# Optimization experiments

Measured on AMD Instinct MI355X. Metric: run time of the kernel, lower is better.

Reference implementation:

```python
import jax, jax.numpy as jnp
import numpy as np

FIELD_NUM = 40
EMBED_DIM = 64
BATCH = 2048

# pair indices matching itertools.combinations(range(F), 2) order
_I, _J = np.triu_indices(FIELD_NUM, k=1)
PAIR_I = jnp.asarray(_I)
PAIR_J = jnp.asarray(_J)


def setup_inputs() -> dict:
    key = jax.random.key(0)
    k1, k2 = jax.random.split(key)
    inputs = jax.random.normal(k1, (BATCH, FIELD_NUM, EMBED_DIM), dtype=jnp.float32)
    # glorot_normal for square [D, D] weight: std = sqrt(2 / (D + D)) = sqrt(1/D)
    w = jax.random.normal(k2, (EMBED_DIM, EMBED_DIM), dtype=jnp.float32) * (1.0 / EMBED_DIM) ** 0.5
    return {"inputs": inputs, "w": w}


def reference(inputs, w):
    # inputs: [B, F, D], w: [D, D]
    # bilinear_type='all': p_{ij} = (v_i @ W) * v_j for all i<j, concat on feature axis
    xw = jnp.einsum("bfd,de->bfe", inputs, w)          # [B, F, D] (one GEMM, shared W)
    p = xw[:, PAIR_I, :] * inputs[:, PAIR_J, :]          # [B, P, D], P = F*(F-1)/2
    B = inputs.shape[0]
    return p.reshape(B, -1)                               # [B, P*D] == tf.concat(p, axis=1)
```

## Files before the change

kernel.cpp:

```cpp
#include <hip/hip_runtime.h>

#define FNUM 40
#define DIM  64
#define NPAIR 780
#define BLOCK 256
#define IN4   (FNUM * DIM / 4)
#define OUT4  (NPAIR * DIM / 4)

typedef float f32x4 __attribute__((ext_vector_type(4)));

__global__ __launch_bounds__(BLOCK)
void bilinear_fused(const float* __restrict__ in,
                    const float* __restrict__ w,
                    float* __restrict__ out)
{
    __shared__ float sIn[FNUM * DIM];
    __shared__ float sXW[FNUM * DIM];
    __shared__ unsigned char sPi[NPAIR];
    __shared__ unsigned char sPj[NPAIR];

    const int tid  = threadIdx.x;
    const int b    = blockIdx.x;
    const int lane = tid & 63;
    const int wv   = tid >> 6;

    const f32x4* in4 = (const f32x4*)in + (size_t)b * IN4;
    f32x4* sIn4 = (f32x4*)sIn;
    for (int k = tid; k < IN4; k += BLOCK) sIn4[k] = in4[k];

    if (tid < FNUM) {
        int i = tid;
        int off = i * (2 * FNUM - 1 - i) / 2;
        for (int j = i + 1; j < FNUM; ++j) {
            sPi[off] = (unsigned char)i;
            sPj[off] = (unsigned char)j;
            ++off;
        }
    }

    float wcol[DIM];
    #pragma unroll
    for (int d = 0; d < DIM; ++d) wcol[d] = w[d * DIM + lane];

    __syncthreads();

    for (int r = 0; r < 10; ++r) {
        int f = wv * 10 + r;
        float rin = sIn[f * DIM + lane];
        float acc = 0.f;
        #pragma unroll
        for (int d = 0; d < DIM; ++d) {
            float bv = __uint_as_float(
                __builtin_amdgcn_readlane(__float_as_uint(rin), d));
            acc = fmaf(bv, wcol[d], acc);
        }
        sXW[f * DIM + lane] = acc;
    }

    __syncthreads();

    const f32x4* sXW4 = (const f32x4*)sXW;
    f32x4* out4 = (f32x4*)out + (size_t)b * OUT4;
    for (int idx = tid; idx < OUT4; idx += BLOCK) {
        int p = idx >> 4;
        int q = idx & 15;
        int i = sPi[p];
        int j = sPj[p];
        f32x4 a = sXW4[i * 16 + q];
        f32x4 v = sIn4[j * 16 + q];
        out4[idx] = a * v;
    }
}

extern "C" void kernel_launch(void* const* d_in, const int* in_sizes, int n_in,
                              void* d_out, int out_size, void* d_ws, size_t ws_size,
                              hipStream_t stream)
{
    const float* in = (const float*)d_in[0];
    const float* w  = (const float*)d_in[1];
    float* out = (float*)d_out;

    bilinear_fused<<<2048, BLOCK, 0, stream>>>(in, w, out);
}
```

Baseline: 421.0 us.

## Split fused kernel into GEMM pass and chunked pair-product streaming pass

Breaks the fused kernel in two. The first kernel writes the XW product to workspace. The second kernel splits each batch row's 780 pair outputs across 4 blocks, which gives four times as many blocks streaming the large output write. It reads operands from global memory or cache instead of LDS and computes pair indices with a sqrt formula instead of a lookup table. The cost is an extra global round trip for xw and a second launch. If workspace is too small it falls back to the original fused kernel.

```diff
diff --git a/kernel.cpp b/kernel.cpp
--- a/kernel.cpp
+++ b/kernel.cpp
@@ -6,8 +6,84 @@
 #define BLOCK 256
 #define IN4   (FNUM * DIM / 4)
 #define OUT4  (NPAIR * DIM / 4)
+#define XWF   (FNUM * DIM)
+#define CHUNKS 4
+#define PPC   (NPAIR / CHUNKS)
+#define C4    (PPC * DIM / 4)
+#define BATCH 2048
 
 typedef float f32x4 __attribute__((ext_vector_type(4)));
+
+#define PAIR_IJ(p, i, j)                                               \
+    int i = (int)((79.0f - sqrtf((float)(6241 - 8 * (p)))) * 0.5f);    \
+    int _off = (i * (79 - i)) >> 1;                                    \
+    if ((p) < _off) { --i; _off = (i * (79 - i)) >> 1; }               \
+    else { int _o2 = ((i + 1) * (78 - i)) >> 1;                        \
+           if ((p) >= _o2) { ++i; _off = _o2; } }                      \
+    int j = i + 1 + ((p) - _off)
+
+__global__ __launch_bounds__(BLOCK)
+void gemm_xw(const float* __restrict__ in,
+             const float* __restrict__ w,
+             float* __restrict__ xw)
+{
+    const int tid  = threadIdx.x;
+    const int b    = blockIdx.x;
+    const int lane = tid & 63;
+    const int wv   = tid >> 6;
+
+    const float* __restrict__ inb = in + (size_t)b * XWF;
+    float*       __restrict__ xwb = xw + (size_t)b * XWF;
+
+    float wcol[DIM];
+    #pragma unroll
+    for (int d = 0; d < DIM; ++d) wcol[d] = w[d * DIM + lane];
+
+    for (int r = 0; r < 10; ++r) {
+        int f = wv * 10 + r;
+        float rin = inb[f * DIM + lane];
+        float acc = 0.f;
+        #pragma unroll
+        for (int d = 0; d < DIM; ++d) {
+            float bv = __uint_as_float(
+                __builtin_amdgcn_readlane(__float_as_uint(rin), d));
+            acc = fmaf(bv, wcol[d], acc);
+        }
+        xwb[f * DIM + lane] = acc;
+    }
+}
+
+__global__ __launch_bounds__(BLOCK)
+void pair_stream(const float* __restrict__ in,
+                 const float* __restrict__ xw,
+                 float* __restrict__ out)
+{
+    const int tid = threadIdx.x;
+    const int b   = blockIdx.x >> 2;
+    const int c   = blockIdx.x & 3;
+
+    const f32x4* __restrict__ in4 = (const f32x4*)in + (size_t)b * IN4;
+    const f32x4* __restrict__ xw4 = (const f32x4*)xw + (size_t)b * IN4;
+    f32x4*       __restrict__ o4  = (f32x4*)out + (size_t)b * OUT4 + (size_t)c * C4;
+
+    const int q     = tid & 15;
+    const int pbase = c * PPC;
+    const int prel0 = tid >> 4;
+
+    #pragma unroll 4
+    for (int k = 0; k < 12; ++k) {
+        int il = tid + k * BLOCK;
+        int p  = pbase + prel0 + k * 16;
+        PAIR_IJ(p, i, j);
+        o4[il] = xw4[i * 16 + q] * in4[j * 16 + q];
+    }
+    if (tid < 48) {
+        int il = tid + 12 * BLOCK;
+        int p  = pbase + prel0 + 12 * 16;
+        PAIR_IJ(p, i, j);
+        o4[il] = xw4[i * 16 + q] * in4[j * 16 + q];
+    }
+}
 
 __global__ __launch_bounds__(BLOCK)
 void bilinear_fused(const float* __restrict__ in,
@@ -63,12 +139,10 @@
     f32x4* out4 = (f32x4*)out + (size_t)b * OUT4;
     for (int idx = tid; idx < OUT4; idx += BLOCK) {
         int p = idx >> 4;
-        int q = idx & 15;
+        int qq = idx & 15;
         int i = sPi[p];
         int j = sPj[p];
-        f32x4 a = sXW4[i * 16 + q];
-        f32x4 v = sIn4[j * 16 + q];
-        out4[idx] = a * v;
+        out4[idx] = sXW4[i * 16 + qq] * sIn4[j * 16 + qq];
     }
 }
 
@@ -80,5 +154,12 @@
     const float* w  = (const float*)d_in[1];
     float* out = (float*)d_out;
 
-    bilinear_fused<<<2048, BLOCK, 0, stream>>>(in, w, out);
+    const size_t need = (size_t)BATCH * XWF * sizeof(float);
+    if (d_ws != nullptr && ws_size >= need) {
+        float* xw = (float*)d_ws;
+        gemm_xw<<<BATCH, BLOCK, 0, stream>>>(in, w, xw);
+        pair_stream<<<BATCH * CHUNKS, BLOCK, 0, stream>>>(in, xw, out);
+    } else {
+        bilinear_fused<<<BATCH, BLOCK, 0, stream>>>(in, w, out);
+    }
 }
```

Result: slower. 472.2 us (+12.2%).
